# Performance work log

Hardware: AMD Instinct MI355X
Metric: run time of the kernel (lower is better)

The kernel has to match this reference:

```python
import jax, jax.numpy as jnp
import numpy as np


def _sage_conv(x_src, x_dst, src, dst, W_l, b_l, W_r):
    """PyG SAGEConv (mean aggr): lin_l(mean_{j in N(i)} x_j) + lin_r(x_i)."""
    n_dst = x_dst.shape[0]
    agg = jax.ops.segment_sum(x_src[src], dst, num_segments=n_dst)  # [n_dst, d]
    cnt = jax.ops.segment_sum(jnp.ones((src.shape[0],), x_src.dtype), dst,
                              num_segments=n_dst)
    mean = agg / jnp.maximum(cnt, 1.0)[:, None]  # mean=0 for isolated targets
    return mean @ W_l.T + b_l + x_dst @ W_r.T


def setup_inputs() -> dict:
    key = jax.random.key(0)
    ks = jax.random.split(key, 12)
    N0, N1, N2, D = 500000, 50000, 5000, 128
    E1, E2 = 1000000, 50000
    s = 1.0 / np.sqrt(D)  # kaiming-uniform-ish init scale, fan_in=128 everywhere
    return {
        "x": jax.random.normal(ks[0], (N0, D), jnp.float32),
        "W1_l": jax.random.uniform(ks[1], (128, D), jnp.float32, -s, s),
        "b1_l": jax.random.uniform(ks[2], (128,), jnp.float32, -s, s),
        "W1_r": jax.random.uniform(ks[3], (128, D), jnp.float32, -s, s),
        "W2_l": jax.random.uniform(ks[4], (64, 128), jnp.float32, -s, s),
        "b2_l": jax.random.uniform(ks[5], (64,), jnp.float32, -s, s),
        "W2_r": jax.random.uniform(ks[6], (64, 128), jnp.float32, -s, s),
        "src1": jax.random.randint(ks[7], (E1,), 0, N0, jnp.int32),
        "dst1": jax.random.randint(ks[8], (E1,), 0, N1, jnp.int32),
        "src2": jax.random.randint(ks[9], (E2,), 0, N1, jnp.int32),
        "dst2": jax.random.randint(ks[10], (E2,), 0, N2, jnp.int32),
        "size1": N1,
        "size2": N2,
    }


def reference(x, W1_l, b1_l, W1_r, W2_l, b2_l, W2_r,
              src1, dst1, src2, dst2, size1, size2):
    # Layer 1: bipartite SAGEConv over sampled edges; dropout is identity (eval)
    h = _sage_conv(x, x[:size1], src1, dst1, W1_l, b1_l, W1_r)
    h = jax.nn.relu(h)  # [size1, 128]
    # Layer 2
    h2 = _sage_conv(h, h[:size2], src2, dst2, W2_l, b2_l, W2_r)
    return jax.nn.relu(h2)  # [size2, 64]
```

## Files before the change

### kernel.cpp

```cpp
#include <hip/hip_runtime.h>
#include <cstdint>
#include <cstddef>

#define DFEAT 128
#define H1 128
#define H2 64
#define N1C 50000
#define N2C 5000
#define CAP1 96
#define CAP2 64

typedef __attribute__((ext_vector_type(8))) __bf16 bf16x8;
typedef __attribute__((ext_vector_type(4))) float f32x4;
typedef unsigned short ushort_t;
typedef unsigned int uint_t;

__device__ __forceinline__ uint_t f2bf(float f) {
    uint_t x = __float_as_uint(f);
    return (x + 0x7fffu + ((x >> 16) & 1u)) >> 16;
}

__device__ __forceinline__ bf16x8 pack8(float4 lo, float4 hi) {
    union { uint_t u[4]; bf16x8 v; } r;
    r.u[0] = f2bf(lo.x) | (f2bf(lo.y) << 16);
    r.u[1] = f2bf(lo.z) | (f2bf(lo.w) << 16);
    r.u[2] = f2bf(hi.x) | (f2bf(hi.y) << 16);
    r.u[3] = f2bf(hi.z) | (f2bf(hi.w) << 16);
    return r.v;
}

__global__ __launch_bounds__(256) void prep(
    const float* __restrict__ W1l, const float* __restrict__ W1r,
    const float* __restrict__ W2l, const float* __restrict__ W2r,
    ushort_t* __restrict__ Wtt1, ushort_t* __restrict__ Wtt2,
    int* __restrict__ cnt1, int* __restrict__ cnt2)
{
    int i = blockIdx.x * 256 + threadIdx.x;
    if (i < N1C) { cnt1[i] = 0; return; }
    i -= N1C;
    if (i < N2C) { cnt2[i] = 0; return; }
    i -= N2C;
    if (i < H1 * 256) {
        int o = i >> 8, k = i & 255;
        Wtt1[i] = (ushort_t)f2bf(k < 128 ? W1l[o * 128 + k] : W1r[o * 128 + (k - 128)]);
        return;
    }
    i -= H1 * 256;
    if (i < H2 * 256) {
        int o = i >> 8, k = i & 255;
        Wtt2[i] = (ushort_t)f2bf(k < 128 ? W2l[o * 128 + k] : W2r[o * 128 + (k - 128)]);
    }
}

__global__ __launch_bounds__(256) void scatter_append(
    const int* __restrict__ src1, const int* __restrict__ dst1, int E1,
    int* __restrict__ cnt1, int* __restrict__ b1,
    const int* __restrict__ src2, const int* __restrict__ dst2, int E2,
    int* __restrict__ cnt2, int* __restrict__ b2)
{
    int tid = blockIdx.x * 256 + threadIdx.x;
    if (tid < E1) {
        int d = dst1[tid];
        int p = atomicAdd(&cnt1[d], 1);
        if (p < CAP1) b1[(size_t)d * CAP1 + p] = src1[tid];
    } else if (tid - E1 < E2) {
        int e = tid - E1;
        int d = dst2[e];
        int p = atomicAdd(&cnt2[d], 1);
        if (p < CAP2) b2[(size_t)d * CAP2 + p] = src2[e];
    }
}

template <int CAP, bool SRC_F32>
__global__ __launch_bounds__(256) void aggregate(
    const void* __restrict__ xsrc_,
    const int* __restrict__ cnt,
    const int* __restrict__ bucket,
    ushort_t* __restrict__ meanb,
    int n_dst)
{
    int t = threadIdx.x, lane = t & 63, wid = t >> 6;
    int n = blockIdx.x * 4 + wid;
    if (n >= n_dst) return;
    int deg = cnt[n];
    if (deg > CAP) deg = CAP;
    const int* row = bucket + (size_t)n * CAP;
    float ax = 0.f, ay = 0.f;
    int j = 0;
    if constexpr (SRC_F32) {
        const float* xb = (const float*)xsrc_ + lane * 2;
        for (; j + 4 <= deg; j += 4) {
            int s0 = row[j], s1 = row[j + 1], s2 = row[j + 2], s3 = row[j + 3];
            float2 v0 = *reinterpret_cast<const float2*>(xb + (size_t)s0 * DFEAT);
            float2 v1 = *reinterpret_cast<const float2*>(xb + (size_t)s1 * DFEAT);
            float2 v2 = *reinterpret_cast<const float2*>(xb + (size_t)s2 * DFEAT);
            float2 v3 = *reinterpret_cast<const float2*>(xb + (size_t)s3 * DFEAT);
            ax += v0.x + v1.x + v2.x + v3.x;
            ay += v0.y + v1.y + v2.y + v3.y;
        }
        for (; j < deg; ++j) {
            float2 v = *reinterpret_cast<const float2*>(xb + (size_t)row[j] * DFEAT);
            ax += v.x; ay += v.y;
        }
    } else {
        const ushort_t* xs = (const ushort_t*)xsrc_;
        auto rowld = [&](int sid) -> uint_t {
            return reinterpret_cast<const uint_t*>(xs + (size_t)sid * DFEAT)[lane];
        };
        auto accum = [&](uint_t v) {
            ax += __uint_as_float((v & 0xffffu) << 16);
            ay += __uint_as_float(v & 0xffff0000u);
        };
        for (; j + 4 <= deg; j += 4) {
            uint_t v0 = rowld(row[j]), v1 = rowld(row[j + 1]);
            uint_t v2 = rowld(row[j + 2]), v3 = rowld(row[j + 3]);
            accum(v0); accum(v1); accum(v2); accum(v3);
        }
        for (; j < deg; ++j) accum(rowld(row[j]));
    }
    float inv = 1.f / fmaxf((float)deg, 1.f);
    uint_t p = f2bf(ax * inv) | (f2bf(ay * inv) << 16);
    reinterpret_cast<uint_t*>(meanb + (size_t)n * DFEAT)[lane] = p;
}

template <int DOUT, bool XDST_F32, bool OUT_BF16>
__global__ __launch_bounds__(256) void sage_mfma(
    const ushort_t* __restrict__ meanb,
    const void* __restrict__ xdst_,
    const ushort_t* __restrict__ Wtt,
    const float* __restrict__ bias,
    void* __restrict__ outp,
    int n_dst)
{
    constexpr int NT = DOUT / 16;
    int t = threadIdx.x, lane = t & 63, wid = t >> 6;
    int m0 = (blockIdx.x * 4 + wid) * 16;
    if (m0 >= n_dst) return;

    int arow = m0 + (lane & 15);
    if (arow >= n_dst) arow = n_dst - 1;
    int kg = (lane >> 4) * 8;

    bf16x8 a[8];
    #pragma unroll
    for (int ks = 0; ks < 4; ++ks)
        a[ks] = *reinterpret_cast<const bf16x8*>(meanb + (size_t)arow * 128 + ks * 32 + kg);
    if constexpr (XDST_F32) {
        const float* xr = (const float*)xdst_ + (size_t)arow * 128 + kg;
        #pragma unroll
        for (int ks = 0; ks < 4; ++ks) {
            float4 lo = *reinterpret_cast<const float4*>(xr + ks * 32);
            float4 hi = *reinterpret_cast<const float4*>(xr + ks * 32 + 4);
            a[4 + ks] = pack8(lo, hi);
        }
    } else {
        const ushort_t* xr = (const ushort_t*)xdst_;
        #pragma unroll
        for (int ks = 0; ks < 4; ++ks)
            a[4 + ks] = *reinterpret_cast<const bf16x8*>(xr + (size_t)arow * 128 + ks * 32 + kg);
    }

    f32x4 acc[NT];
    #pragma unroll
    for (int nt = 0; nt < NT; ++nt) {
        acc[nt] = (f32x4){0.f, 0.f, 0.f, 0.f};
        const ushort_t* wrow = Wtt + (size_t)(nt * 16 + (lane & 15)) * 256 + kg;
        #pragma unroll
        for (int ks = 0; ks < 8; ++ks) {
            bf16x8 b = *reinterpret_cast<const bf16x8*>(wrow + ks * 32);
            acc[nt] = __builtin_amdgcn_mfma_f32_16x16x32_bf16(a[ks], b, acc[nt], 0, 0, 0);
        }
    }

    int col = lane & 15;
    int r0 = (lane >> 4) * 4;
    #pragma unroll
    for (int nt = 0; nt < NT; ++nt) {
        int o = nt * 16 + col;
        float bv = bias[o];
        #pragma unroll
        for (int j = 0; j < 4; ++j) {
            int node = m0 + r0 + j;
            if (node < n_dst) {
                float v = fmaxf(acc[nt][j] + bv, 0.f);
                if constexpr (OUT_BF16)
                    ((ushort_t*)outp)[(size_t)node * DOUT + o] = (ushort_t)f2bf(v);
                else
                    ((float*)outp)[(size_t)node * DOUT + o] = v;
            }
        }
    }
}

extern "C" void kernel_launch(void* const* d_in, const int* in_sizes, int n_in,
                              void* d_out, int out_size, void* d_ws, size_t ws_size,
                              hipStream_t stream) {
    const float* x   = (const float*)d_in[0];
    const float* W1l = (const float*)d_in[1];
    const float* b1  = (const float*)d_in[2];
    const float* W1r = (const float*)d_in[3];
    const float* W2l = (const float*)d_in[4];
    const float* b2  = (const float*)d_in[5];
    const float* W2r = (const float*)d_in[6];
    const int* src1  = (const int*)d_in[7];
    const int* dst1  = (const int*)d_in[8];
    const int* src2  = (const int*)d_in[9];
    const int* dst2  = (const int*)d_in[10];
    const int E1 = in_sizes[7];
    const int E2 = in_sizes[9];
    const int n1 = N1C, n2 = N2C;

    char* w = (char*)d_ws;
    auto carve = [&](size_t bytes) {
        char* p = w;
        w += (bytes + 255) & ~(size_t)255;
        return p;
    };
    int* cnt1       = (int*)carve((size_t)n1 * 4);
    int* cnt2       = (int*)carve((size_t)n2 * 4);
    int* b1k        = (int*)carve((size_t)n1 * CAP1 * 4);
    int* b2k        = (int*)carve((size_t)n2 * CAP2 * 4);
    ushort_t* Wtt1  = (ushort_t*)carve((size_t)H1 * 256 * 2);
    ushort_t* Wtt2  = (ushort_t*)carve((size_t)H2 * 256 * 2);
    ushort_t* mean1 = (ushort_t*)carve((size_t)n1 * DFEAT * 2);
    ushort_t* mean2 = (ushort_t*)carve((size_t)n2 * DFEAT * 2);
    ushort_t* h     = (ushort_t*)carve((size_t)n1 * H1 * 2);

    {
        int total = n1 + n2 + H1 * 256 + H2 * 256;
        prep<<<(total + 255) / 256, 256, 0, stream>>>(W1l, W1r, W2l, W2r,
                                                      Wtt1, Wtt2, cnt1, cnt2);
    }
    {
        int total = E1 + E2;
        scatter_append<<<(total + 255) / 256, 256, 0, stream>>>(
            src1, dst1, E1, cnt1, b1k, src2, dst2, E2, cnt2, b2k);
    }
    aggregate<CAP1, true><<<(n1 + 3) / 4, 256, 0, stream>>>(x, cnt1, b1k, mean1, n1);
    {
        int waves = (n1 + 15) / 16;
        sage_mfma<H1, true, true><<<(waves + 3) / 4, 256, 0, stream>>>(
            mean1, x, Wtt1, b1, h, n1);
    }
    aggregate<CAP2, false><<<(n2 + 3) / 4, 256, 0, stream>>>(h, cnt2, b2k, mean2, n2);
    {
        int waves = (n2 + 15) / 16;
        sage_mfma<H2, false, false><<<(waves + 3) / 4, 256, 0, stream>>>(
            mean2, h, Wtt2, b2, d_out, n2);
    }
}
```

Before: 211.7 us.

## Pre-convert x to bf16 and fuse neighbor aggregation with MFMA projection

Adds a pass that converts the whole 500k x 128 fp32 feature matrix to bf16, folded into the edge-bucketing kernel. Both layers now use one fused kernel: each block gathers the neighbor means for 16 nodes into shared memory, then runs the MFMA projection with the output tiles split across its waves. This removes the mean intermediates and two launches, and halves the bytes per gathered row. In exchange it streams all of x once and writes a 128MB bf16 copy even for rows that are never gathered, and it rounds layer-1 inputs to bf16 before averaging.

```diff
diff --git a/kernel.cpp b/kernel.cpp
--- a/kernel.cpp
+++ b/kernel.cpp
@@ -5,6 +5,7 @@
 #define DFEAT 128
 #define H1 128
 #define H2 64
+#define N0C 500000
 #define N1C 50000
 #define N2C 5000
 #define CAP1 96
@@ -19,14 +20,8 @@
     uint_t x = __float_as_uint(f);
     return (x + 0x7fffu + ((x >> 16) & 1u)) >> 16;
 }
-
-__device__ __forceinline__ bf16x8 pack8(float4 lo, float4 hi) {
-    union { uint_t u[4]; bf16x8 v; } r;
-    r.u[0] = f2bf(lo.x) | (f2bf(lo.y) << 16);
-    r.u[1] = f2bf(lo.z) | (f2bf(lo.w) << 16);
-    r.u[2] = f2bf(hi.x) | (f2bf(hi.y) << 16);
-    r.u[3] = f2bf(hi.z) | (f2bf(hi.w) << 16);
-    return r.v;
+__device__ __forceinline__ uint_t pack2(float a, float b) {
+    return f2bf(a) | (f2bf(b) << 16);
 }
 
 __global__ __launch_bounds__(256) void prep(
@@ -52,7 +47,8 @@
     }
 }
 
-__global__ __launch_bounds__(256) void scatter_append(
+__global__ __launch_bounds__(256) void convert_scatter(
+    const float* __restrict__ x, ushort_t* __restrict__ xb,
     const int* __restrict__ src1, const int* __restrict__ dst1, int E1,
     int* __restrict__ cnt1, int* __restrict__ b1,
     const int* __restrict__ src2, const int* __restrict__ dst2, int E2,
@@ -63,126 +59,113 @@
         int d = dst1[tid];
         int p = atomicAdd(&cnt1[d], 1);
         if (p < CAP1) b1[(size_t)d * CAP1 + p] = src1[tid];
-    } else if (tid - E1 < E2) {
-        int e = tid - E1;
-        int d = dst2[e];
+        return;
+    }
+    tid -= E1;
+    if (tid < E2) {
+        int d = dst2[tid];
         int p = atomicAdd(&cnt2[d], 1);
-        if (p < CAP2) b2[(size_t)d * CAP2 + p] = src2[e];
-    }
-}
-
-template <int CAP, bool SRC_F32>
-__global__ __launch_bounds__(256) void aggregate(
-    const void* __restrict__ xsrc_,
+        if (p < CAP2) b2[(size_t)d * CAP2 + p] = src2[tid];
+        return;
+    }
+    tid -= E2;
+    constexpr int NCONV = N0C * DFEAT / 8;
+    if (tid < NCONV) {
+        const float4* xin = reinterpret_cast<const float4*>(x);
+        float4 v0 = xin[(size_t)tid * 2];
+        float4 v1 = xin[(size_t)tid * 2 + 1];
+        uint4 o;
+        o.x = pack2(v0.x, v0.y); o.y = pack2(v0.z, v0.w);
+        o.z = pack2(v1.x, v1.y); o.w = pack2(v1.z, v1.w);
+        reinterpret_cast<uint4*>(xb)[tid] = o;
+    }
+}
+
+template <int DOUT, int CAP, bool OUT_BF16>
+__global__ __launch_bounds__(256) void sage_fused(
+    const ushort_t* __restrict__ xsrc,
+    const ushort_t* __restrict__ xdst,
     const int* __restrict__ cnt,
     const int* __restrict__ bucket,
-    ushort_t* __restrict__ meanb,
-    int n_dst)
-{
-    int t = threadIdx.x, lane = t & 63, wid = t >> 6;
-    int n = blockIdx.x * 4 + wid;
-    if (n >= n_dst) return;
-    int deg = cnt[n];
-    if (deg > CAP) deg = CAP;
-    const int* row = bucket + (size_t)n * CAP;
-    float ax = 0.f, ay = 0.f;
-    int j = 0;
-    if constexpr (SRC_F32) {
-        const float* xb = (const float*)xsrc_ + lane * 2;
-        for (; j + 4 <= deg; j += 4) {
-            int s0 = row[j], s1 = row[j + 1], s2 = row[j + 2], s3 = row[j + 3];
-            float2 v0 = *reinterpret_cast<const float2*>(xb + (size_t)s0 * DFEAT);
-            float2 v1 = *reinterpret_cast<const float2*>(xb + (size_t)s1 * DFEAT);
-            float2 v2 = *reinterpret_cast<const float2*>(xb + (size_t)s2 * DFEAT);
-            float2 v3 = *reinterpret_cast<const float2*>(xb + (size_t)s3 * DFEAT);
-            ax += v0.x + v1.x + v2.x + v3.x;
-            ay += v0.y + v1.y + v2.y + v3.y;
-        }
-        for (; j < deg; ++j) {
-            float2 v = *reinterpret_cast<const float2*>(xb + (size_t)row[j] * DFEAT);
-            ax += v.x; ay += v.y;
-        }
-    } else {
-        const ushort_t* xs = (const ushort_t*)xsrc_;
-        auto rowld = [&](int sid) -> uint_t {
-            return reinterpret_cast<const uint_t*>(xs + (size_t)sid * DFEAT)[lane];
-        };
-        auto accum = [&](uint_t v) {
-            ax += __uint_as_float((v & 0xffffu) << 16);
-            ay += __uint_as_float(v & 0xffff0000u);
-        };
-        for (; j + 4 <= deg; j += 4) {
-            uint_t v0 = rowld(row[j]), v1 = rowld(row[j + 1]);
-            uint_t v2 = rowld(row[j + 2]), v3 = rowld(row[j + 3]);
-            accum(v0); accum(v1); accum(v2); accum(v3);
-        }
-        for (; j < deg; ++j) accum(rowld(row[j]));
-    }
-    float inv = 1.f / fmaxf((float)deg, 1.f);
-    uint_t p = f2bf(ax * inv) | (f2bf(ay * inv) << 16);
-    reinterpret_cast<uint_t*>(meanb + (size_t)n * DFEAT)[lane] = p;
-}
-
-template <int DOUT, bool XDST_F32, bool OUT_BF16>
-__global__ __launch_bounds__(256) void sage_mfma(
-    const ushort_t* __restrict__ meanb,
-    const void* __restrict__ xdst_,
     const ushort_t* __restrict__ Wtt,
     const float* __restrict__ bias,
     void* __restrict__ outp,
     int n_dst)
 {
+    __shared__ ushort_t u[16][136];
+    int t = threadIdx.x, lane = t & 63, wid = t >> 6;
+    int node0 = blockIdx.x * 16;
+
+    auto rowld = [&](int sid) -> uint_t {
+        return reinterpret_cast<const uint_t*>(xsrc + (size_t)sid * DFEAT)[lane];
+    };
+    for (int i = 0; i < 4; ++i) {
+        int nl = wid * 4 + i;
+        int n = node0 + nl;
+        float ax = 0.f, ay = 0.f;
+        int deg = 0;
+        if (n < n_dst) {
+            deg = cnt[n];
+            if (deg > CAP) deg = CAP;
+            const int* row = bucket + (size_t)n * CAP;
+            auto bacc = [&](uint_t v) {
+                ax += __uint_as_float(v << 16);
+                ay += __uint_as_float(v & 0xffff0000u);
+            };
+            int j = 0;
+            for (; j + 8 <= deg; j += 8) {
+                int4 q0 = *reinterpret_cast<const int4*>(row + j);
+                int4 q1 = *reinterpret_cast<const int4*>(row + j + 4);
+                uint_t v0 = rowld(q0.x), v1 = rowld(q0.y), v2 = rowld(q0.z), v3 = rowld(q0.w);
+                uint_t v4 = rowld(q1.x), v5 = rowld(q1.y), v6 = rowld(q1.z), v7 = rowld(q1.w);
+                bacc(v0); bacc(v1); bacc(v2); bacc(v3);
+                bacc(v4); bacc(v5); bacc(v6); bacc(v7);
+            }
+            if (j + 4 <= deg) {
+                int4 q = *reinterpret_cast<const int4*>(row + j);
+                uint_t v0 = rowld(q.x), v1 = rowld(q.y), v2 = rowld(q.z), v3 = rowld(q.w);
+                bacc(v0); bacc(v1); bacc(v2); bacc(v3);
+                j += 4;
+            }
+            for (; j < deg; ++j) bacc(rowld(row[j]));
+        }
+        float inv = 1.f / fmaxf((float)deg, 1.f);
+        *reinterpret_cast<uint_t*>(&u[nl][lane * 2]) = pack2(ax * inv, ay * inv);
+    }
+    __syncthreads();
+
     constexpr int NT = DOUT / 16;
-    int t = threadIdx.x, lane = t & 63, wid = t >> 6;
-    int m0 = (blockIdx.x * 4 + wid) * 16;
-    if (m0 >= n_dst) return;
-
-    int arow = m0 + (lane & 15);
-    if (arow >= n_dst) arow = n_dst - 1;
+    constexpr int TPW = NT / 4;
+    int r = lane & 15;
     int kg = (lane >> 4) * 8;
-
     bf16x8 a[8];
     #pragma unroll
     for (int ks = 0; ks < 4; ++ks)
-        a[ks] = *reinterpret_cast<const bf16x8*>(meanb + (size_t)arow * 128 + ks * 32 + kg);
-    if constexpr (XDST_F32) {
-        const float* xr = (const float*)xdst_ + (size_t)arow * 128 + kg;
-        #pragma unroll
-        for (int ks = 0; ks < 4; ++ks) {
-            float4 lo = *reinterpret_cast<const float4*>(xr + ks * 32);
-            float4 hi = *reinterpret_cast<const float4*>(xr + ks * 32 + 4);
-            a[4 + ks] = pack8(lo, hi);
-        }
-    } else {
-        const ushort_t* xr = (const ushort_t*)xdst_;
-        #pragma unroll
-        for (int ks = 0; ks < 4; ++ks)
-            a[4 + ks] = *reinterpret_cast<const bf16x8*>(xr + (size_t)arow * 128 + ks * 32 + kg);
-    }
-
-    f32x4 acc[NT];
+        a[ks] = *reinterpret_cast<const bf16x8*>(&u[r][ks * 32 + kg]);
+    int garow = node0 + r;
+    if (garow >= n_dst) garow = n_dst - 1;
     #pragma unroll
-    for (int nt = 0; nt < NT; ++nt) {
-        acc[nt] = (f32x4){0.f, 0.f, 0.f, 0.f};
-        const ushort_t* wrow = Wtt + (size_t)(nt * 16 + (lane & 15)) * 256 + kg;
+    for (int ks = 0; ks < 4; ++ks)
+        a[4 + ks] = *reinterpret_cast<const bf16x8*>(xdst + (size_t)garow * 128 + ks * 32 + kg);
+
+    int r0 = (lane >> 4) * 4;
+    #pragma unroll
+    for (int tp = 0; tp < TPW; ++tp) {
+        int nt = wid * TPW + tp;
+        f32x4 acc = (f32x4){0.f, 0.f, 0.f, 0.f};
+        const ushort_t* wrow = Wtt + (size_t)(nt * 16 + r) * 256 + kg;
         #pragma unroll
         for (int ks = 0; ks < 8; ++ks) {
             bf16x8 b = *reinterpret_cast<const bf16x8*>(wrow + ks * 32);
-            acc[nt] = __builtin_amdgcn_mfma_f32_16x16x32_bf16(a[ks], b, acc[nt], 0, 0, 0);
+            acc = __builtin_amdgcn_mfma_f32_16x16x32_bf16(a[ks], b, acc, 0, 0, 0);
         }
-    }
-
-    int col = lane & 15;
-    int r0 = (lane >> 4) * 4;
-    #pragma unroll
-    for (int nt = 0; nt < NT; ++nt) {
-        int o = nt * 16 + col;
+        int o = nt * 16 + r;
         float bv = bias[o];
         #pragma unroll
-        for (int j = 0; j < 4; ++j) {
-            int node = m0 + r0 + j;
+        for (int jj = 0; jj < 4; ++jj) {
+            int node = node0 + r0 + jj;
             if (node < n_dst) {
-                float v = fmaxf(acc[nt][j] + bv, 0.f);
+                float v = fmaxf(acc[jj] + bv, 0.f);
                 if constexpr (OUT_BF16)
                     ((ushort_t*)outp)[(size_t)node * DOUT + o] = (ushort_t)f2bf(v);
                 else
@@ -222,8 +205,7 @@
     int* b2k        = (int*)carve((size_t)n2 * CAP2 * 4);
     ushort_t* Wtt1  = (ushort_t*)carve((size_t)H1 * 256 * 2);
     ushort_t* Wtt2  = (ushort_t*)carve((size_t)H2 * 256 * 2);
-    ushort_t* mean1 = (ushort_t*)carve((size_t)n1 * DFEAT * 2);
-    ushort_t* mean2 = (ushort_t*)carve((size_t)n2 * DFEAT * 2);
+    ushort_t* xb    = (ushort_t*)carve((size_t)N0C * DFEAT * 2);
     ushort_t* h     = (ushort_t*)carve((size_t)n1 * H1 * 2);
 
     {
@@ -232,20 +214,12 @@
                                                       Wtt1, Wtt2, cnt1, cnt2);
     }
     {
-        int total = E1 + E2;
-        scatter_append<<<(total + 255) / 256, 256, 0, stream>>>(
-            src1, dst1, E1, cnt1, b1k, src2, dst2, E2, cnt2, b2k);
-    }
-    aggregate<CAP1, true><<<(n1 + 3) / 4, 256, 0, stream>>>(x, cnt1, b1k, mean1, n1);
-    {
-        int waves = (n1 + 15) / 16;
-        sage_mfma<H1, true, true><<<(waves + 3) / 4, 256, 0, stream>>>(
-            mean1, x, Wtt1, b1, h, n1);
-    }
-    aggregate<CAP2, false><<<(n2 + 3) / 4, 256, 0, stream>>>(h, cnt2, b2k, mean2, n2);
-    {
-        int waves = (n2 + 15) / 16;
-        sage_mfma<H2, false, false><<<(waves + 3) / 4, 256, 0, stream>>>(
-            mean2, h, Wtt2, b2, d_out, n2);
-    }
-}
+        long long total = (long long)E1 + E2 + (long long)N0C * DFEAT / 8;
+        convert_scatter<<<(int)((total + 255) / 256), 256, 0, stream>>>(
+            x, xb, src1, dst1, E1, cnt1, b1k, src2, dst2, E2, cnt2, b2k);
+    }
+    sage_fused<H1, CAP1, true><<<(n1 + 15) / 16, 256, 0, stream>>>(
+        xb, xb, cnt1, b1k, Wtt1, b1, h, n1);
+    sage_fused<H2, CAP2, false><<<(n2 + 15) / 16, 256, 0, stream>>>(
+        h, h, cnt2, b2k, Wtt2, b2, d_out, n2);
+}
```

Result: slower. 231.6 us (+9.4%).
